# Optimization experiments

Measured on AMD Instinct MI355X. Metric: run time of the kernel, lower is better.

The kernel has to match this reference:

```python
import jax, jax.numpy as jnp
import numpy as np

B, T, F, H, E = 32, 512, 64, 64, 32  # batch, time, features(=sequence_length), hidden_dim, encoding_size


def setup_inputs() -> dict:
    key = jax.random.key(0)
    ks = jax.random.split(key, 14)
    sc = 0.05
    return {
        "x": jax.random.normal(ks[0], (B, T, F), jnp.float32),
        "s": jax.random.normal(ks[1], (B, T, E), jnp.float32),
        # gating FFN params
        "ffn_w1": jax.random.normal(ks[2], (F, H), jnp.float32) * sc,
        "ffn_b1": jnp.zeros((H,), jnp.float32),
        "ffn_w2": jax.random.normal(ks[3], (E, H), jnp.float32) * sc,
        "ffn_b2": jnp.zeros((H,), jnp.float32),
        "ffn_w3": jax.random.normal(ks[4], (H, F), jnp.float32) * sc,
        "ffn_b3": jnp.zeros((F,), jnp.float32),
        # per-feature expert FFN_j params (F experts, each Dense(1->H), ELU, Dense(H->H))
        "exp_w1": jax.random.normal(ks[5], (F, H), jnp.float32) * sc,  # weight of Dense(1->H) per feature
        "exp_b1": jnp.zeros((F, H), jnp.float32),
        "exp_w3": jax.random.normal(ks[6], (F, H, H), jnp.float32) * sc,
        "exp_b3": jnp.zeros((F, H), jnp.float32),
    }


def reference(x, s, ffn_w1, ffn_b1, ffn_w2, ffn_b2, ffn_w3, ffn_b3,
              exp_w1, exp_b1, exp_w3, exp_b3):
    # gating network: softmax over feature axis
    g = jnp.einsum('btf,fh->bth', x, ffn_w1) + ffn_b1 \
        + jnp.einsum('bte,eh->bth', s, ffn_w2) + ffn_b2
    logits = jnp.einsum('bth,hf->btf', jax.nn.elu(g), ffn_w3) + ffn_b3
    w_t = jax.nn.softmax(logits, axis=2)  # [B,T,F]

    # per-feature experts, batched: Dense(1->H) is a rank-1 outer product
    h = jax.nn.elu(x[..., None] * exp_w1[None, None] + exp_b1[None, None])  # [B,T,F,H]
    expert_out = jnp.einsum('btfh,fhk->btfk', h, exp_w3) + exp_b3[None, None]  # [B,T,F,H]

    # gate-weighted sum over features
    return jnp.einsum('btfk,btf->btk', expert_out, w_t)  # [B,T,H]
```

## Files before the change

kernel.cpp:

```cpp
#include <hip/hip_runtime.h>
#include <hip/hip_bf16.h>
#include <math.h>

#define NTOK 16384

typedef __attribute__((ext_vector_type(8))) short short8;
typedef __attribute__((ext_vector_type(4))) float f32x4;

__device__ __forceinline__ unsigned pack_bf16(float a, float b) {
    union { __hip_bfloat162 h; unsigned u; } cv;
    cv.h = __float22bfloat162_rn(make_float2(a, b));
    return cv.u;
}
__device__ __forceinline__ float eluf(float z) {
    return z > 0.0f ? z : (__expf(z) - 1.0f);
}

__global__ __launch_bounds__(256)
void prepass(const float* __restrict__ ew3, const float* __restrict__ eb3,
             unsigned short* __restrict__ ws) {
    __shared__ float tile[64 * 65];
    const int bid = blockIdx.x, tid = threadIdx.x;
    const float* src = (bid < 64) ? (ew3 + (size_t)bid * 4096) : eb3;

    const int r = tid >> 2, c0 = (tid & 3) * 16;
    #pragma unroll
    for (int j = 0; j < 4; ++j) {
        float4 v = *(const float4*)(src + r * 64 + c0 + j * 4);
        tile[r * 65 + c0 + j * 4 + 0] = v.x;
        tile[r * 65 + c0 + j * 4 + 1] = v.y;
        tile[r * 65 + c0 + j * 4 + 2] = v.z;
        tile[r * 65 + c0 + j * 4 + 3] = v.w;
    }
    __syncthreads();

    uint4* dst = (uint4*)(ws + (size_t)bid * 4096);
    #pragma unroll
    for (int it = 0; it < 2; ++it) {
        const int idx = tid + it * 256;
        const int c = idx >> 8, u = (idx >> 6) & 3, l = idx & 63;
        const int m = l & 15, q = (l >> 4) & 3;
        const int rb = c * 32 + q * 8, col = u * 16 + m;
        unsigned pw[4];
        #pragma unroll
        for (int p = 0; p < 4; ++p)
            pw[p] = pack_bf16(tile[(rb + 2 * p) * 65 + col],
                              tile[(rb + 2 * p + 1) * 65 + col]);
        uint4 pk; pk.x = pw[0]; pk.y = pw[1]; pk.z = pw[2]; pk.w = pw[3];
        dst[idx] = pk;
    }
}

__global__ __launch_bounds__(512, 4)
void moe_main(const float* __restrict__ x,   const float* __restrict__ s,
              const float* __restrict__ fw1, const float* __restrict__ fb1,
              const float* __restrict__ fw2, const float* __restrict__ fb2,
              const float* __restrict__ fw3, const float* __restrict__ fb3,
              const float* __restrict__ ew1, const float* __restrict__ eb1,
              const float* __restrict__ ew3, const float* __restrict__ eb3,
              const unsigned short* __restrict__ img,
              float* __restrict__ out)
{
    __shared__ __align__(16) float xls[32 * 68];
    __shared__ __align__(16) float wts[32 * 65];
    __shared__ __align__(16) float egs[32 * 64];
    __shared__ __align__(16) float ped0[4][16 * 68];
    __shared__ __align__(16) float ped1[4][16 * 68];

    const int tid = threadIdx.x;
    const int wv = tid >> 6, lane = tid & 63;
    const int m = tid & 15, quad = (tid >> 4) & 3;
    const int tokbase = blockIdx.x * 32;

    {
        const int t = tid >> 4, fq = (tid & 15) * 4;
        *(float4*)&xls[t * 68 + fq] =
            *(const float4*)(x + (size_t)(tokbase + t) * 64 + fq);
    }
    __syncthreads();

    {
        const int t0w = wv * 4;
        const float* sw = s + (size_t)(tokbase + t0w) * 32;
        float g[4];
        const float b0 = fb1[lane] + fb2[lane];
        #pragma unroll
        for (int t = 0; t < 4; ++t) g[t] = b0;
        for (int f = 0; f < 64; f += 4) {
            const float w0 = fw1[(f + 0) * 64 + lane];
            const float w1 = fw1[(f + 1) * 64 + lane];
            const float w2 = fw1[(f + 2) * 64 + lane];
            const float w3v = fw1[(f + 3) * 64 + lane];
            #pragma unroll
            for (int t = 0; t < 4; ++t) {
                const float4 xa = *(const float4*)&xls[(t0w + t) * 68 + f];
                g[t] = fmaf(xa.x, w0, fmaf(xa.y, w1, fmaf(xa.z, w2, fmaf(xa.w, w3v, g[t]))));
            }
        }
        for (int e = 0; e < 32; e += 4) {
            const float w0 = fw2[(e + 0) * 64 + lane];
            const float w1 = fw2[(e + 1) * 64 + lane];
            const float w2 = fw2[(e + 2) * 64 + lane];
            const float w3v = fw2[(e + 3) * 64 + lane];
            #pragma unroll
            for (int t = 0; t < 4; ++t) {
                const float4 sa = *(const float4*)(sw + t * 32 + e);
                g[t] = fmaf(sa.x, w0, fmaf(sa.y, w1, fmaf(sa.z, w2, fmaf(sa.w, w3v, g[t]))));
            }
        }
        #pragma unroll
        for (int t = 0; t < 4; ++t) egs[(t0w + t) * 64 + lane] = eluf(g[t]);

        float lg[4];
        const float b3 = fb3[lane];
        #pragma unroll
        for (int t = 0; t < 4; ++t) lg[t] = b3;
        for (int h = 0; h < 64; h += 4) {
            const float w0 = fw3[(h + 0) * 64 + lane];
            const float w1 = fw3[(h + 1) * 64 + lane];
            const float w2 = fw3[(h + 2) * 64 + lane];
            const float w3v = fw3[(h + 3) * 64 + lane];
            #pragma unroll
            for (int t = 0; t < 4; ++t) {
                const float4 ev = *(const float4*)&egs[(t0w + t) * 64 + h];
                lg[t] = fmaf(ev.x, w0, fmaf(ev.y, w1, fmaf(ev.z, w2, fmaf(ev.w, w3v, lg[t]))));
            }
        }
        #pragma unroll
        for (int t = 0; t < 4; ++t) {
            float mx = lg[t];
            #pragma unroll
            for (int off = 32; off > 0; off >>= 1) mx = fmaxf(mx, __shfl_xor(mx, off));
            const float p = __expf(lg[t] - mx);
            float sm = p;
            #pragma unroll
            for (int off = 32; off > 0; off >>= 1) sm += __shfl_xor(sm, off);
            wts[(t0w + t) * 65 + lane] = p / sm;
        }
    }
    __syncthreads();

    const int f0 = wv * 8;
    f32x4 acc0[4], acc1[4];
    #pragma unroll
    for (int u = 0; u < 4; ++u) {
        acc0[u] = (f32x4){0.f, 0.f, 0.f, 0.f};
        acc1[u] = (f32x4){0.f, 0.f, 0.f, 0.f};
    }

    const uint4* bp = (const uint4*)img + (size_t)f0 * 512 + lane;
    uint4  B[2][8];
    float4 W[2][4];
    float4 Bb[2][4];
    float  XV[2][2];
    float  WT[2][2];

    #pragma unroll
    for (int i = 0; i < 8; ++i) B[0][i] = bp[(i >> 2) * 256 + (i & 3) * 64];
    bp += 512;
    #pragma unroll
    for (int c = 0; c < 2; ++c) {
        W[0][c * 2 + 0]  = *(const float4*)(ew1 + f0 * 64 + c * 32 + quad * 8);
        W[0][c * 2 + 1]  = *(const float4*)(ew1 + f0 * 64 + c * 32 + quad * 8 + 4);
        Bb[0][c * 2 + 0] = *(const float4*)(eb1 + f0 * 64 + c * 32 + quad * 8);
        Bb[0][c * 2 + 1] = *(const float4*)(eb1 + f0 * 64 + c * 32 + quad * 8 + 4);
    }
    XV[0][0] = xls[m * 68 + f0];        WT[0][0] = wts[m * 65 + f0];
    XV[0][1] = xls[(16 + m) * 68 + f0]; WT[0][1] = wts[(16 + m) * 65 + f0];

    #pragma unroll
    for (int ff = 0; ff < 8; ++ff) {
        const int cur = ff & 1, nxt = cur ^ 1;
        if (ff < 7) {
            const int fn = f0 + ff + 1;
            #pragma unroll
            for (int i = 0; i < 8; ++i) B[nxt][i] = bp[(i >> 2) * 256 + (i & 3) * 64];
            bp += 512;
            #pragma unroll
            for (int c = 0; c < 2; ++c) {
                W[nxt][c * 2 + 0]  = *(const float4*)(ew1 + fn * 64 + c * 32 + quad * 8);
                W[nxt][c * 2 + 1]  = *(const float4*)(ew1 + fn * 64 + c * 32 + quad * 8 + 4);
                Bb[nxt][c * 2 + 0] = *(const float4*)(eb1 + fn * 64 + c * 32 + quad * 8);
                Bb[nxt][c * 2 + 1] = *(const float4*)(eb1 + fn * 64 + c * 32 + quad * 8 + 4);
            }
            XV[nxt][0] = xls[m * 68 + fn];        WT[nxt][0] = wts[m * 65 + fn];
            XV[nxt][1] = xls[(16 + m) * 68 + fn]; WT[nxt][1] = wts[(16 + m) * 65 + fn];
        }
        const float xv0 = XV[cur][0], wt0 = WT[cur][0];
        const float xv1 = XV[cur][1], wt1 = WT[cur][1];
        short8 a0[2], a1[2];
        #pragma unroll
        for (int c = 0; c < 2; ++c) {
            const float4 wa = W[cur][c * 2 + 0],  wb = W[cur][c * 2 + 1];
            const float4 ba = Bb[cur][c * 2 + 0], bb = Bb[cur][c * 2 + 1];
            uint4 v0, v1;
            v0.x = pack_bf16(wt0 * eluf(fmaf(xv0, wa.x, ba.x)),
                             wt0 * eluf(fmaf(xv0, wa.y, ba.y)));
            v0.y = pack_bf16(wt0 * eluf(fmaf(xv0, wa.z, ba.z)),
                             wt0 * eluf(fmaf(xv0, wa.w, ba.w)));
            v0.z = pack_bf16(wt0 * eluf(fmaf(xv0, wb.x, bb.x)),
                             wt0 * eluf(fmaf(xv0, wb.y, bb.y)));
            v0.w = pack_bf16(wt0 * eluf(fmaf(xv0, wb.z, bb.z)),
                             wt0 * eluf(fmaf(xv0, wb.w, bb.w)));
            v1.x = pack_bf16(wt1 * eluf(fmaf(xv1, wa.x, ba.x)),
                             wt1 * eluf(fmaf(xv1, wa.y, ba.y)));
            v1.y = pack_bf16(wt1 * eluf(fmaf(xv1, wa.z, ba.z)),
                             wt1 * eluf(fmaf(xv1, wa.w, ba.w)));
            v1.z = pack_bf16(wt1 * eluf(fmaf(xv1, wb.x, bb.x)),
                             wt1 * eluf(fmaf(xv1, wb.y, bb.y)));
            v1.w = pack_bf16(wt1 * eluf(fmaf(xv1, wb.z, bb.z)),
                             wt1 * eluf(fmaf(xv1, wb.w, bb.w)));
            a0[c] = *(short8*)&v0;
            a1[c] = *(short8*)&v1;
        }
        acc0[0] = __builtin_amdgcn_mfma_f32_16x16x32_bf16(a0[0], *(short8*)&B[cur][0], acc0[0], 0, 0, 0);
        acc0[1] = __builtin_amdgcn_mfma_f32_16x16x32_bf16(a0[0], *(short8*)&B[cur][1], acc0[1], 0, 0, 0);
        acc0[2] = __builtin_amdgcn_mfma_f32_16x16x32_bf16(a0[0], *(short8*)&B[cur][2], acc0[2], 0, 0, 0);
        acc0[3] = __builtin_amdgcn_mfma_f32_16x16x32_bf16(a0[0], *(short8*)&B[cur][3], acc0[3], 0, 0, 0);
        acc1[0] = __builtin_amdgcn_mfma_f32_16x16x32_bf16(a1[0], *(short8*)&B[cur][0], acc1[0], 0, 0, 0);
        acc1[1] = __builtin_amdgcn_mfma_f32_16x16x32_bf16(a1[0], *(short8*)&B[cur][1], acc1[1], 0, 0, 0);
        acc1[2] = __builtin_amdgcn_mfma_f32_16x16x32_bf16(a1[0], *(short8*)&B[cur][2], acc1[2], 0, 0, 0);
        acc1[3] = __builtin_amdgcn_mfma_f32_16x16x32_bf16(a1[0], *(short8*)&B[cur][3], acc1[3], 0, 0, 0);
        acc0[0] = __builtin_amdgcn_mfma_f32_16x16x32_bf16(a0[1], *(short8*)&B[cur][4], acc0[0], 0, 0, 0);
        acc0[1] = __builtin_amdgcn_mfma_f32_16x16x32_bf16(a0[1], *(short8*)&B[cur][5], acc0[1], 0, 0, 0);
        acc0[2] = __builtin_amdgcn_mfma_f32_16x16x32_bf16(a0[1], *(short8*)&B[cur][6], acc0[2], 0, 0, 0);
        acc0[3] = __builtin_amdgcn_mfma_f32_16x16x32_bf16(a0[1], *(short8*)&B[cur][7], acc0[3], 0, 0, 0);
        acc1[0] = __builtin_amdgcn_mfma_f32_16x16x32_bf16(a1[1], *(short8*)&B[cur][4], acc1[0], 0, 0, 0);
        acc1[1] = __builtin_amdgcn_mfma_f32_16x16x32_bf16(a1[1], *(short8*)&B[cur][5], acc1[1], 0, 0, 0);
        acc1[2] = __builtin_amdgcn_mfma_f32_16x16x32_bf16(a1[1], *(short8*)&B[cur][6], acc1[2], 0, 0, 0);
        acc1[3] = __builtin_amdgcn_mfma_f32_16x16x32_bf16(a1[1], *(short8*)&B[cur][7], acc1[3], 0, 0, 0);
    }

    if (wv < 4) {
        const int tile = wv >> 1, eh = wv & 1;
        const int e0 = eh * 32 + quad * 8;
        const int trow = tile * 16 + m;
        uint4 av;
        av.x = pack_bf16(wts[trow * 65 + e0 + 0], wts[trow * 65 + e0 + 1]);
        av.y = pack_bf16(wts[trow * 65 + e0 + 2], wts[trow * 65 + e0 + 3]);
        av.z = pack_bf16(wts[trow * 65 + e0 + 4], wts[trow * 65 + e0 + 5]);
        av.w = pack_bf16(wts[trow * 65 + e0 + 6], wts[trow * 65 + e0 + 7]);
        short8 a = *(short8*)&av;
        const uint4* bq = (const uint4*)img + (size_t)64 * 512;
        if (tile == 0) {
            #pragma unroll
            for (int u = 0; u < 4; ++u) {
                uint4 bv = bq[eh * 256 + u * 64 + lane];
                acc0[u] = __builtin_amdgcn_mfma_f32_16x16x32_bf16(a, *(short8*)&bv, acc0[u], 0, 0, 0);
            }
        } else {
            #pragma unroll
            for (int u = 0; u < 4; ++u) {
                uint4 bv = bq[eh * 256 + u * 64 + lane];
                acc1[u] = __builtin_amdgcn_mfma_f32_16x16x32_bf16(a, *(short8*)&bv, acc1[u], 0, 0, 0);
            }
        }
    }

    if (wv >= 4) {
        #pragma unroll
        for (int u = 0; u < 4; ++u)
            #pragma unroll
            for (int r = 0; r < 4; ++r) {
                const int idx = (quad * 4 + r) * 68 + u * 16 + m;
                ped0[wv - 4][idx] = acc0[u][r];
                ped1[wv - 4][idx] = acc1[u][r];
            }
    }
    __syncthreads();
    if (wv < 4) {
        #pragma unroll
        for (int u = 0; u < 4; ++u)
            #pragma unroll
            for (int r = 0; r < 4; ++r) {
                const int idx = (quad * 4 + r) * 68 + u * 16 + m;
                acc0[u][r] += ped0[wv][idx];
                acc1[u][r] += ped1[wv][idx];
            }
    }
    __syncthreads();
    if (wv == 2 || wv == 3) {
        #pragma unroll
        for (int u = 0; u < 4; ++u)
            #pragma unroll
            for (int r = 0; r < 4; ++r) {
                const int idx = (quad * 4 + r) * 68 + u * 16 + m;
                ped0[wv - 2][idx] = acc0[u][r];
                ped1[wv - 2][idx] = acc1[u][r];
            }
    }
    __syncthreads();
    if (wv < 2) {
        #pragma unroll
        for (int u = 0; u < 4; ++u)
            #pragma unroll
            for (int r = 0; r < 4; ++r) {
                const int idx = (quad * 4 + r) * 68 + u * 16 + m;
                acc0[u][r] += ped0[wv][idx];
                acc1[u][r] += ped1[wv][idx];
            }
    }
    __syncthreads();
    if (wv == 1) {
        #pragma unroll
        for (int u = 0; u < 4; ++u)
            #pragma unroll
            for (int r = 0; r < 4; ++r) {
                const int idx = (quad * 4 + r) * 68 + u * 16 + m;
                ped0[0][idx] = acc0[u][r];
                ped1[0][idx] = acc1[u][r];
            }
    }
    __syncthreads();
    if (wv == 0) {
        #pragma unroll
        for (int u = 0; u < 4; ++u)
            #pragma unroll
            for (int r = 0; r < 4; ++r) {
                const int idx = (quad * 4 + r) * 68 + u * 16 + m;
                ped0[0][idx] += acc0[u][r];
                ped1[0][idx] += acc1[u][r];
            }
    }
    __syncthreads();

    {
        const int t = tid >> 4, kq = tid & 15;
        const float* srcp = (t < 16) ? &ped0[0][t * 68 + kq * 4]
                                     : &ped1[0][(t - 16) * 68 + kq * 4];
        *(float4*)(out + (size_t)(tokbase + t) * 64 + kq * 4) = *(const float4*)srcp;
    }
}

__device__ __forceinline__ void gen_a_fb(const float* __restrict__ ew1,
                                         const float* __restrict__ eb1,
                                         int f, int quad, float xv, float wt,
                                         short8* a) {
    #pragma unroll
    for (int c = 0; c < 2; ++c) {
        const float* w1p = ew1 + f * 64 + c * 32 + quad * 8;
        const float* b1p = eb1 + f * 64 + c * 32 + quad * 8;
        const float4 w1a = *(const float4*)w1p, w1b = *(const float4*)(w1p + 4);
        const float4 b1a = *(const float4*)b1p, b1b = *(const float4*)(b1p + 4);
        uint4 av;
        av.x = pack_bf16(wt * eluf(fmaf(xv, w1a.x, b1a.x)),
                         wt * eluf(fmaf(xv, w1a.y, b1a.y)));
        av.y = pack_bf16(wt * eluf(fmaf(xv, w1a.z, b1a.z)),
                         wt * eluf(fmaf(xv, w1a.w, b1a.w)));
        av.z = pack_bf16(wt * eluf(fmaf(xv, w1b.x, b1b.x)),
                         wt * eluf(fmaf(xv, w1b.y, b1b.y)));
        av.w = pack_bf16(wt * eluf(fmaf(xv, w1b.z, b1b.z)),
                         wt * eluf(fmaf(xv, w1b.w, b1b.w)));
        a[c] = *(short8*)&av;
    }
}
__device__ __forceinline__ void gen_b_fp32(const float* __restrict__ w3f,
                                           int quad, int m, short8 b[2][4]) {
    #pragma unroll
    for (int c = 0; c < 2; ++c)
        #pragma unroll
        for (int u = 0; u < 4; ++u) {
            const float* wp = w3f + (size_t)(c * 32 + quad * 8) * 64 + u * 16 + m;
            uint4 v;
            v.x = pack_bf16(wp[0],   wp[64]);
            v.y = pack_bf16(wp[128], wp[192]);
            v.z = pack_bf16(wp[256], wp[320]);
            v.w = pack_bf16(wp[384], wp[448]);
            b[c][u] = *(short8*)&v;
        }
}

__global__ __launch_bounds__(512, 8)
void moe_fb(const float* __restrict__ x,   const float* __restrict__ s,
            const float* __restrict__ fw1, const float* __restrict__ fb1,
            const float* __restrict__ fw2, const float* __restrict__ fb2,
            const float* __restrict__ fw3, const float* __restrict__ fb3,
            const float* __restrict__ ew1, const float* __restrict__ eb1,
            const float* __restrict__ ew3, const float* __restrict__ eb3,
            float* __restrict__ out)
{
    __shared__ __align__(16) float xls[16 * 68];
    __shared__ __align__(16) float wts[16 * 65];
    __shared__ __align__(16) float egs[16 * 64];
    __shared__ __align__(16) float ped[4][16 * 68];

    const int tid = threadIdx.x;
    const int wv = tid >> 6, lane = tid & 63;
    const int tokbase = blockIdx.x * 16;

    if (tid < 256) {
        const int t = tid >> 4, fq = (tid & 15) * 4;
        *(float4*)&xls[t * 68 + fq] =
            *(const float4*)(x + (size_t)(tokbase + t) * 64 + fq);
    }
    __syncthreads();
    {
        const int t0w = wv * 2;
        const float* sw = s + (size_t)(tokbase + t0w) * 32;
        float g0, g1;
        g0 = g1 = fb1[lane] + fb2[lane];
        for (int ff = 0; ff < 64; ff += 4) {
            const float4 xa = *(const float4*)&xls[(t0w + 0) * 68 + ff];
            const float4 xb = *(const float4*)&xls[(t0w + 1) * 68 + ff];
            const float w0 = fw1[(ff + 0) * 64 + lane];
            const float w1 = fw1[(ff + 1) * 64 + lane];
            const float w2 = fw1[(ff + 2) * 64 + lane];
            const float w3v = fw1[(ff + 3) * 64 + lane];
            g0 = fmaf(xa.x, w0, fmaf(xa.y, w1, fmaf(xa.z, w2, fmaf(xa.w, w3v, g0))));
            g1 = fmaf(xb.x, w0, fmaf(xb.y, w1, fmaf(xb.z, w2, fmaf(xb.w, w3v, g1))));
        }
        for (int e = 0; e < 32; e += 4) {
            const float4 sa = *(const float4*)(sw + e);
            const float4 sb = *(const float4*)(sw + 32 + e);
            const float w0 = fw2[(e + 0) * 64 + lane];
            const float w1 = fw2[(e + 1) * 64 + lane];
            const float w2 = fw2[(e + 2) * 64 + lane];
            const float w3v = fw2[(e + 3) * 64 + lane];
            g0 = fmaf(sa.x, w0, fmaf(sa.y, w1, fmaf(sa.z, w2, fmaf(sa.w, w3v, g0))));
            g1 = fmaf(sb.x, w0, fmaf(sb.y, w1, fmaf(sb.z, w2, fmaf(sb.w, w3v, g1))));
        }
        egs[(t0w + 0) * 64 + lane] = eluf(g0);
        egs[(t0w + 1) * 64 + lane] = eluf(g1);
        float lg0 = fb3[lane], lg1 = lg0;
        for (int h = 0; h < 64; h += 4) {
            const float4 e0 = *(const float4*)&egs[(t0w + 0) * 64 + h];
            const float4 e1 = *(const float4*)&egs[(t0w + 1) * 64 + h];
            const float w0 = fw3[(h + 0) * 64 + lane];
            const float w1 = fw3[(h + 1) * 64 + lane];
            const float w2 = fw3[(h + 2) * 64 + lane];
            const float w3v = fw3[(h + 3) * 64 + lane];
            lg0 = fmaf(e0.x, w0, fmaf(e0.y, w1, fmaf(e0.z, w2, fmaf(e0.w, w3v, lg0))));
            lg1 = fmaf(e1.x, w0, fmaf(e1.y, w1, fmaf(e1.z, w2, fmaf(e1.w, w3v, lg1))));
        }
        float mx0 = lg0, mx1 = lg1;
        #pragma unroll
        for (int off = 32; off > 0; off >>= 1) {
            mx0 = fmaxf(mx0, __shfl_xor(mx0, off));
            mx1 = fmaxf(mx1, __shfl_xor(mx1, off));
        }
        const float p0 = __expf(lg0 - mx0), p1 = __expf(lg1 - mx1);
        float s0 = p0, s1 = p1;
        #pragma unroll
        for (int off = 32; off > 0; off >>= 1) {
            s0 += __shfl_xor(s0, off);
            s1 += __shfl_xor(s1, off);
        }
        wts[(t0w + 0) * 65 + lane] = p0 / s0;
        wts[(t0w + 1) * 65 + lane] = p1 / s1;
    }
    __syncthreads();

    const int m = tid & 15, quad = (tid >> 4) & 3;
    const int f0 = wv * 8;
    f32x4 acc[4];
    #pragma unroll
    for (int u = 0; u < 4; ++u) acc[u] = (f32x4){0.f, 0.f, 0.f, 0.f};

    #pragma unroll
    for (int ff = 0; ff < 8; ++ff) {
        const int fcur = f0 + ff;
        short8 b[2][4], a[2];
        gen_b_fp32(ew3 + (size_t)fcur * 4096, quad, m, b);
        gen_a_fb(ew1, eb1, fcur, quad, xls[m * 68 + fcur], wts[m * 65 + fcur], a);
        #pragma unroll
        for (int u = 0; u < 4; ++u) {
            acc[u] = __builtin_amdgcn_mfma_f32_16x16x32_bf16(a[0], b[0][u], acc[u], 0, 0, 0);
            acc[u] = __builtin_amdgcn_mfma_f32_16x16x32_bf16(a[1], b[1][u], acc[u], 0, 0, 0);
        }
    }
    if (wv < 2) {
        const int e0 = wv * 32 + quad * 8;
        uint4 av;
        av.x = pack_bf16(wts[m * 65 + e0 + 0], wts[m * 65 + e0 + 1]);
        av.y = pack_bf16(wts[m * 65 + e0 + 2], wts[m * 65 + e0 + 3]);
        av.z = pack_bf16(wts[m * 65 + e0 + 4], wts[m * 65 + e0 + 5]);
        av.w = pack_bf16(wts[m * 65 + e0 + 6], wts[m * 65 + e0 + 7]);
        short8 a = *(short8*)&av;
        #pragma unroll
        for (int u = 0; u < 4; ++u) {
            const float* wp = eb3 + (size_t)e0 * 64 + u * 16 + m;
            uint4 bv;
            bv.x = pack_bf16(wp[0],   wp[64]);
            bv.y = pack_bf16(wp[128], wp[192]);
            bv.z = pack_bf16(wp[256], wp[320]);
            bv.w = pack_bf16(wp[384], wp[448]);
            acc[u] = __builtin_amdgcn_mfma_f32_16x16x32_bf16(a, *(short8*)&bv, acc[u], 0, 0, 0);
        }
    }
    if (wv >= 4) {
        #pragma unroll
        for (int u = 0; u < 4; ++u)
            #pragma unroll
            for (int r = 0; r < 4; ++r)
                ped[wv - 4][(quad * 4 + r) * 68 + u * 16 + m] = acc[u][r];
    }
    __syncthreads();
    if (wv < 4) {
        #pragma unroll
        for (int u = 0; u < 4; ++u)
            #pragma unroll
            for (int r = 0; r < 4; ++r)
                acc[u][r] += ped[wv][(quad * 4 + r) * 68 + u * 16 + m];
    }
    __syncthreads();
    if (wv == 2 || wv == 3) {
        #pragma unroll
        for (int u = 0; u < 4; ++u)
            #pragma unroll
            for (int r = 0; r < 4; ++r)
                ped[wv - 2][(quad * 4 + r) * 68 + u * 16 + m] = acc[u][r];
    }
    __syncthreads();
    if (wv < 2) {
        #pragma unroll
        for (int u = 0; u < 4; ++u)
            #pragma unroll
            for (int r = 0; r < 4; ++r)
                acc[u][r] += ped[wv][(quad * 4 + r) * 68 + u * 16 + m];
    }
    __syncthreads();
    if (wv == 1) {
        #pragma unroll
        for (int u = 0; u < 4; ++u)
            #pragma unroll
            for (int r = 0; r < 4; ++r)
                ped[0][(quad * 4 + r) * 68 + u * 16 + m] = acc[u][r];
    }
    __syncthreads();
    if (wv == 0) {
        #pragma unroll
        for (int u = 0; u < 4; ++u)
            #pragma unroll
            for (int r = 0; r < 4; ++r)
                ped[0][(quad * 4 + r) * 68 + u * 16 + m] += acc[u][r];
    }
    __syncthreads();
    if (tid < 256) {
        const int t = tid >> 4, kq = tid & 15;
        float4 o = *(const float4*)&ped[0][t * 68 + kq * 4];
        *(float4*)(out + (size_t)(tokbase + t) * 64 + kq * 4) = o;
    }
}

extern "C" void kernel_launch(void* const* d_in, const int* in_sizes, int n_in,
                              void* d_out, int out_size, void* d_ws, size_t ws_size,
                              hipStream_t stream) {
    const float* x   = (const float*)d_in[0];
    const float* s   = (const float*)d_in[1];
    const float* fw1 = (const float*)d_in[2];
    const float* fb1 = (const float*)d_in[3];
    const float* fw2 = (const float*)d_in[4];
    const float* fb2 = (const float*)d_in[5];
    const float* fw3 = (const float*)d_in[6];
    const float* fb3 = (const float*)d_in[7];
    const float* ew1 = (const float*)d_in[8];
    const float* eb1 = (const float*)d_in[9];
    const float* ew3 = (const float*)d_in[10];
    const float* eb3 = (const float*)d_in[11];
    float* out = (float*)d_out;

    const size_t ws_need = (size_t)65 * 4096 * sizeof(unsigned short);
    if (ws_size >= ws_need && (((uintptr_t)d_ws & 15) == 0)) {
        unsigned short* img = (unsigned short*)d_ws;
        prepass<<<dim3(65), dim3(256), 0, stream>>>(ew3, eb3, img);
        moe_main<<<dim3(NTOK / 32), dim3(512), 0, stream>>>(
            x, s, fw1, fb1, fw2, fb2, fw3, fb3, ew1, eb1, ew3, eb3, img, out);
    } else {
        moe_fb<<<dim3(NTOK / 16), dim3(512), 0, stream>>>(
            x, s, fw1, fb1, fw2, fb2, fw3, fb3, ew1, eb1, ew3, eb3, out);
    }
}
```

Before: 116.4 us.

## Split gating softmax into prepass kernel and slim expert MFMA kernel

Moves the gating network (two dense layers, ELU, softmax) into a separate kernel that also converts the expert weights to bf16, writing per-token gate weights to workspace. A new smaller main kernel (256 threads, 16 tokens per block) reads x and the precomputed gates, builds gate-scaled ELU activations in registers, and runs bf16 MFMAs over 16 features per wave, then reduces across waves through shared memory. The intent is to shrink the main kernel's shared memory and register pressure for better occupancy. The cost is an extra round trip of a 4 MB gate tensor through global memory.

```diff
diff --git a/kernel.cpp b/kernel.cpp
--- a/kernel.cpp
+++ b/kernel.cpp
@@ -39,8 +39,8 @@
     for (int it = 0; it < 2; ++it) {
         const int idx = tid + it * 256;
         const int c = idx >> 8, u = (idx >> 6) & 3, l = idx & 63;
-        const int m = l & 15, q = (l >> 4) & 3;
-        const int rb = c * 32 + q * 8, col = u * 16 + m;
+        const int mm = l & 15, q = (l >> 4) & 3;
+        const int rb = c * 32 + q * 8, col = u * 16 + mm;
         unsigned pw[4];
         #pragma unroll
         for (int p = 0; p < 4; ++p)
@@ -48,6 +48,266 @@
                               tile[(rb + 2 * p + 1) * 65 + col]);
         uint4 pk; pk.x = pw[0]; pk.y = pw[1]; pk.z = pw[2]; pk.w = pw[3];
         dst[idx] = pk;
+    }
+}
+
+__global__ __launch_bounds__(256)
+void prep_gate(const float* __restrict__ ew3, const float* __restrict__ eb3,
+               const float* __restrict__ x,   const float* __restrict__ s,
+               const float* __restrict__ fw1, const float* __restrict__ fb1,
+               const float* __restrict__ fw2, const float* __restrict__ fb2,
+               const float* __restrict__ fw3, const float* __restrict__ fb3,
+               unsigned short* __restrict__ img, float* __restrict__ wtg)
+{
+    __shared__ float smem[64 * 65];
+    const int tid = threadIdx.x;
+
+    if (blockIdx.x < 65) {
+        const int bid = blockIdx.x;
+        const float* src = (bid < 64) ? (ew3 + (size_t)bid * 4096) : eb3;
+        const int r = tid >> 2, c0 = (tid & 3) * 16;
+        #pragma unroll
+        for (int j = 0; j < 4; ++j) {
+            float4 v = *(const float4*)(src + r * 64 + c0 + j * 4);
+            smem[r * 65 + c0 + j * 4 + 0] = v.x;
+            smem[r * 65 + c0 + j * 4 + 1] = v.y;
+            smem[r * 65 + c0 + j * 4 + 2] = v.z;
+            smem[r * 65 + c0 + j * 4 + 3] = v.w;
+        }
+        __syncthreads();
+        uint4* dst = (uint4*)(img + (size_t)bid * 4096);
+        #pragma unroll
+        for (int it = 0; it < 2; ++it) {
+            const int idx = tid + it * 256;
+            const int c = idx >> 8, u = (idx >> 6) & 3, l = idx & 63;
+            const int mm = l & 15, q = (l >> 4) & 3;
+            const int rb = c * 32 + q * 8, col = u * 16 + mm;
+            unsigned pw[4];
+            #pragma unroll
+            for (int p = 0; p < 4; ++p)
+                pw[p] = pack_bf16(smem[(rb + 2 * p) * 65 + col],
+                                  smem[(rb + 2 * p + 1) * 65 + col]);
+            uint4 pk; pk.x = pw[0]; pk.y = pw[1]; pk.z = pw[2]; pk.w = pw[3];
+            dst[idx] = pk;
+        }
+        return;
+    }
+
+    float* xls = smem;
+    float* egs = smem + 16 * 68;
+    const int gb = blockIdx.x - 65;
+    const int tokbase = gb * 16;
+    const int wv = tid >> 6, lane = tid & 63;
+
+    {
+        const int t = tid >> 4, fq = (tid & 15) * 4;
+        *(float4*)&xls[t * 68 + fq] =
+            *(const float4*)(x + (size_t)(tokbase + t) * 64 + fq);
+    }
+    __syncthreads();
+
+    const int t0w = wv * 4;
+    const float* sw = s + (size_t)(tokbase + t0w) * 32;
+    float g[4];
+    const float b0 = fb1[lane] + fb2[lane];
+    #pragma unroll
+    for (int t = 0; t < 4; ++t) g[t] = b0;
+    for (int f = 0; f < 64; f += 4) {
+        const float w0 = fw1[(f + 0) * 64 + lane];
+        const float w1 = fw1[(f + 1) * 64 + lane];
+        const float w2 = fw1[(f + 2) * 64 + lane];
+        const float w3v = fw1[(f + 3) * 64 + lane];
+        #pragma unroll
+        for (int t = 0; t < 4; ++t) {
+            const float4 xa = *(const float4*)&xls[(t0w + t) * 68 + f];
+            g[t] = fmaf(xa.x, w0, fmaf(xa.y, w1, fmaf(xa.z, w2, fmaf(xa.w, w3v, g[t]))));
+        }
+    }
+    for (int e = 0; e < 32; e += 4) {
+        const float w0 = fw2[(e + 0) * 64 + lane];
+        const float w1 = fw2[(e + 1) * 64 + lane];
+        const float w2 = fw2[(e + 2) * 64 + lane];
+        const float w3v = fw2[(e + 3) * 64 + lane];
+        #pragma unroll
+        for (int t = 0; t < 4; ++t) {
+            const float4 sa = *(const float4*)(sw + t * 32 + e);
+            g[t] = fmaf(sa.x, w0, fmaf(sa.y, w1, fmaf(sa.z, w2, fmaf(sa.w, w3v, g[t]))));
+        }
+    }
+    #pragma unroll
+    for (int t = 0; t < 4; ++t) egs[(t0w + t) * 64 + lane] = eluf(g[t]);
+
+    float lg[4];
+    const float b3 = fb3[lane];
+    #pragma unroll
+    for (int t = 0; t < 4; ++t) lg[t] = b3;
+    for (int h = 0; h < 64; h += 4) {
+        const float w0 = fw3[(h + 0) * 64 + lane];
+        const float w1 = fw3[(h + 1) * 64 + lane];
+        const float w2 = fw3[(h + 2) * 64 + lane];
+        const float w3v = fw3[(h + 3) * 64 + lane];
+        #pragma unroll
+        for (int t = 0; t < 4; ++t) {
+            const float4 ev = *(const float4*)&egs[(t0w + t) * 64 + h];
+            lg[t] = fmaf(ev.x, w0, fmaf(ev.y, w1, fmaf(ev.z, w2, fmaf(ev.w, w3v, lg[t]))));
+        }
+    }
+    #pragma unroll
+    for (int t = 0; t < 4; ++t) {
+        float mx = lg[t];
+        #pragma unroll
+        for (int off = 32; off > 0; off >>= 1) mx = fmaxf(mx, __shfl_xor(mx, off));
+        const float p = __expf(lg[t] - mx);
+        float sm = p;
+        #pragma unroll
+        for (int off = 32; off > 0; off >>= 1) sm += __shfl_xor(sm, off);
+        wtg[(size_t)(tokbase + t0w + t) * 64 + lane] = p / sm;
+    }
+}
+
+__global__ __launch_bounds__(256, 4)
+void moe_main2(const float* __restrict__ x,
+               const float* __restrict__ ew1, const float* __restrict__ eb1,
+               const unsigned short* __restrict__ img,
+               const float* __restrict__ wtg,
+               float* __restrict__ out)
+{
+    __shared__ __align__(16) float xls[16 * 68];
+    __shared__ __align__(16) float wls[16 * 68];
+    __shared__ __align__(16) float ped[2][16 * 68];
+
+    const int tid = threadIdx.x;
+    const int wv = tid >> 6, lane = tid & 63;
+    const int m = tid & 15, quad = (tid >> 4) & 3;
+    const int tokbase = blockIdx.x * 16;
+
+    {
+        const int t = tid >> 4, fq = (tid & 15) * 4;
+        *(float4*)&xls[t * 68 + fq] =
+            *(const float4*)(x + (size_t)(tokbase + t) * 64 + fq);
+        *(float4*)&wls[t * 68 + fq] =
+            *(const float4*)(wtg + (size_t)(tokbase + t) * 64 + fq);
+    }
+    __syncthreads();
+
+    const int f0 = wv * 16;
+    f32x4 acc[4];
+    #pragma unroll
+    for (int u = 0; u < 4; ++u) acc[u] = (f32x4){0.f, 0.f, 0.f, 0.f};
+
+    const uint4* bp = (const uint4*)img + (size_t)f0 * 512 + lane;
+    float XV[2], WT[2];
+    XV[0] = xls[m * 68 + f0];
+    WT[0] = wls[m * 68 + f0];
+
+    #pragma unroll
+    for (int ff = 0; ff < 16; ++ff) {
+        const int cur = ff & 1, nxt = cur ^ 1;
+        const int fn = f0 + ff;
+
+        uint4 Bv[8];
+        #pragma unroll
+        for (int i = 0; i < 8; ++i) Bv[i] = bp[(i >> 2) * 256 + (i & 3) * 64];
+        bp += 512;
+
+        const float* w1p = ew1 + (size_t)fn * 64 + quad * 8;
+        const float* b1p = eb1 + (size_t)fn * 64 + quad * 8;
+        const float4 wa = *(const float4*)w1p,        wb = *(const float4*)(w1p + 4);
+        const float4 wc = *(const float4*)(w1p + 32), wd = *(const float4*)(w1p + 36);
+        const float4 ba = *(const float4*)b1p,        bbv = *(const float4*)(b1p + 4);
+        const float4 bc = *(const float4*)(b1p + 32), bd = *(const float4*)(b1p + 36);
+
+        if (ff < 15) {
+            XV[nxt] = xls[m * 68 + fn + 1];
+            WT[nxt] = wls[m * 68 + fn + 1];
+        }
+        const float xv = XV[cur], wt = WT[cur];
+
+        uint4 v0, v1;
+        v0.x = pack_bf16(wt * eluf(fmaf(xv, wa.x, ba.x)),
+                         wt * eluf(fmaf(xv, wa.y, ba.y)));
+        v0.y = pack_bf16(wt * eluf(fmaf(xv, wa.z, ba.z)),
+                         wt * eluf(fmaf(xv, wa.w, ba.w)));
+        v0.z = pack_bf16(wt * eluf(fmaf(xv, wb.x, bbv.x)),
+                         wt * eluf(fmaf(xv, wb.y, bbv.y)));
+        v0.w = pack_bf16(wt * eluf(fmaf(xv, wb.z, bbv.z)),
+                         wt * eluf(fmaf(xv, wb.w, bbv.w)));
+        v1.x = pack_bf16(wt * eluf(fmaf(xv, wc.x, bc.x)),
+                         wt * eluf(fmaf(xv, wc.y, bc.y)));
+        v1.y = pack_bf16(wt * eluf(fmaf(xv, wc.z, bc.z)),
+                         wt * eluf(fmaf(xv, wc.w, bc.w)));
+        v1.z = pack_bf16(wt * eluf(fmaf(xv, wd.x, bd.x)),
+                         wt * eluf(fmaf(xv, wd.y, bd.y)));
+        v1.w = pack_bf16(wt * eluf(fmaf(xv, wd.z, bd.z)),
+                         wt * eluf(fmaf(xv, wd.w, bd.w)));
+        const short8 a0 = *(short8*)&v0, a1 = *(short8*)&v1;
+
+        acc[0] = __builtin_amdgcn_mfma_f32_16x16x32_bf16(a0, *(short8*)&Bv[0], acc[0], 0, 0, 0);
+        acc[1] = __builtin_amdgcn_mfma_f32_16x16x32_bf16(a0, *(short8*)&Bv[1], acc[1], 0, 0, 0);
+        acc[2] = __builtin_amdgcn_mfma_f32_16x16x32_bf16(a0, *(short8*)&Bv[2], acc[2], 0, 0, 0);
+        acc[3] = __builtin_amdgcn_mfma_f32_16x16x32_bf16(a0, *(short8*)&Bv[3], acc[3], 0, 0, 0);
+        acc[0] = __builtin_amdgcn_mfma_f32_16x16x32_bf16(a1, *(short8*)&Bv[4], acc[0], 0, 0, 0);
+        acc[1] = __builtin_amdgcn_mfma_f32_16x16x32_bf16(a1, *(short8*)&Bv[5], acc[1], 0, 0, 0);
+        acc[2] = __builtin_amdgcn_mfma_f32_16x16x32_bf16(a1, *(short8*)&Bv[6], acc[2], 0, 0, 0);
+        acc[3] = __builtin_amdgcn_mfma_f32_16x16x32_bf16(a1, *(short8*)&Bv[7], acc[3], 0, 0, 0);
+    }
+
+    if (wv < 2) {
+        const int eh = wv;
+        const int e0 = eh * 32 + quad * 8;
+        uint4 av;
+        av.x = pack_bf16(wls[m * 68 + e0 + 0], wls[m * 68 + e0 + 1]);
+        av.y = pack_bf16(wls[m * 68 + e0 + 2], wls[m * 68 + e0 + 3]);
+        av.z = pack_bf16(wls[m * 68 + e0 + 4], wls[m * 68 + e0 + 5]);
+        av.w = pack_bf16(wls[m * 68 + e0 + 6], wls[m * 68 + e0 + 7]);
+        const short8 a = *(short8*)&av;
+        const uint4* bq = (const uint4*)img + (size_t)64 * 512 + lane;
+        #pragma unroll
+        for (int u = 0; u < 4; ++u) {
+            uint4 bv = bq[eh * 256 + u * 64];
+            acc[u] = __builtin_amdgcn_mfma_f32_16x16x32_bf16(a, *(short8*)&bv, acc[u], 0, 0, 0);
+        }
+    }
+
+    if (wv >= 2) {
+        #pragma unroll
+        for (int u = 0; u < 4; ++u)
+            #pragma unroll
+            for (int r = 0; r < 4; ++r)
+                ped[wv - 2][(quad * 4 + r) * 68 + u * 16 + m] = acc[u][r];
+    }
+    __syncthreads();
+    if (wv < 2) {
+        #pragma unroll
+        for (int u = 0; u < 4; ++u)
+            #pragma unroll
+            for (int r = 0; r < 4; ++r)
+                acc[u][r] += ped[wv][(quad * 4 + r) * 68 + u * 16 + m];
+    }
+    __syncthreads();
+    if (wv == 1) {
+        #pragma unroll
+        for (int u = 0; u < 4; ++u)
+            #pragma unroll
+            for (int r = 0; r < 4; ++r)
+                ped[0][(quad * 4 + r) * 68 + u * 16 + m] = acc[u][r];
+    }
+    __syncthreads();
+    if (wv == 0) {
+        #pragma unroll
+        for (int u = 0; u < 4; ++u)
+            #pragma unroll
+            for (int r = 0; r < 4; ++r) {
+                const int idx = (quad * 4 + r) * 68 + u * 16 + m;
+                ped[1][idx] = acc[u][r] + ped[0][idx];
+            }
+    }
+    __syncthreads();
+
+    {
+        const int t = tid >> 4, kq = tid & 15;
+        *(float4*)(out + (size_t)(tokbase + t) * 64 + kq * 4) =
+            *(const float4*)&ped[1][t * 68 + kq * 4];
     }
 }
 
@@ -559,8 +819,18 @@
     const float* eb3 = (const float*)d_in[11];
     float* out = (float*)d_out;
 
-    const size_t ws_need = (size_t)65 * 4096 * sizeof(unsigned short);
-    if (ws_size >= ws_need && (((uintptr_t)d_ws & 15) == 0)) {
+    const size_t img_bytes = (size_t)65 * 4096 * sizeof(unsigned short);
+    const size_t wt_bytes  = (size_t)NTOK * 64 * sizeof(float);
+    const bool al16 = (((uintptr_t)d_ws & 15) == 0);
+
+    if (ws_size >= img_bytes + wt_bytes && al16) {
+        unsigned short* img = (unsigned short*)d_ws;
+        float* wtg = (float*)((char*)d_ws + img_bytes);
+        prep_gate<<<dim3(65 + NTOK / 16), dim3(256), 0, stream>>>(
+            ew3, eb3, x, s, fw1, fb1, fw2, fb2, fw3, fb3, img, wtg);
+        moe_main2<<<dim3(NTOK / 16), dim3(256), 0, stream>>>(
+            x, ew1, eb1, img, wtg, out);
+    } else if (ws_size >= img_bytes && al16) {
         unsigned short* img = (unsigned short*)d_ws;
         prepass<<<dim3(65), dim3(256), 0, stream>>>(ew3, eb3, img);
         moe_main<<<dim3(NTOK / 32), dim3(512), 0, stream>>>(
```

Result: slower. 128.1 us (+10.0%).
